# Kernel tuning notes

Measured on AMD Instinct MI355X. Metric: run time of the kernel, lower is better.

Reference implementation:

```python
import jax, jax.numpy as jnp
import numpy as np

STRIDE = 16      # image -> feature stride (224 -> 14)
POOL = 7         # ROI pool output grid
FG_HI = 0.85
FG_LO = 0.5


def setup_inputs() -> dict:
    key = jax.random.key(0)
    ks = jax.random.split(key, 8)
    B, N, M, K = 4, 128, 16, 80
    Cf, Tf, Cs, Ts, H, W = 256, 32, 2048, 8, 14, 14
    fast = jax.random.normal(ks[0], (B, Cf, Tf, H, W), jnp.float32)
    slow = jax.random.normal(ks[1], (B, Cs, Ts, H, W), jnp.float32)
    # valid gt boxes inside 224x224
    xy = jax.random.uniform(ks[2], (B, M, 2)) * 160.0
    wh = 32.0 + jax.random.uniform(ks[3], (B, M, 2)) * 48.0
    gt = jnp.concatenate([xy, xy + wh], axis=-1)
    # proposals: first M coincide with gt (guarantees IoU>=0.85 foreground), rest random
    pxy = jax.random.uniform(ks[4], (B, N - M, 2)) * 160.0
    pwh = 16.0 + jax.random.uniform(ks[5], (B, N - M, 2)) * 64.0
    props = jnp.concatenate([gt, jnp.concatenate([pxy, pxy + pwh], axis=-1)], axis=1)
    gt_classes = (jax.random.uniform(ks[6], (B, M, K)) < 0.1).astype(jnp.float32)
    C = Cf + Cs
    W_cls = jax.random.normal(ks[7], (C, K), jnp.float32) * 0.02
    b_cls = jnp.zeros((K,), jnp.float32)
    return dict(fast_feature=fast, slow_feature=slow, proposal_bboxes=props,
                gt_bboxes_batch=gt, gt_classes_batch=gt_classes,
                W_cls=W_cls, b_cls=b_cls)


def _iou(a, b):
    # a: [B,N,4], b: [B,M,4] (x1,y1,x2,y2) -> [B,N,M]
    tl = jnp.maximum(a[:, :, None, :2], b[:, None, :, :2])
    br = jnp.minimum(a[:, :, None, 2:], b[:, None, :, 2:])
    inter = jnp.prod(jnp.clip(br - tl, 0.0), axis=-1)
    area_a = jnp.prod(a[:, :, 2:] - a[:, :, :2], axis=-1)[:, :, None]
    area_b = jnp.prod(b[:, :, 2:] - b[:, :, :2], axis=-1)[:, None, :]
    return inter / (area_a + area_b - inter)


def _roi_pool(feat, boxes):
    # feat: [B,C,H,W]; boxes: [B,N,4] in image coords -> [B,N,P,P,C]
    B, C, H, W = feat.shape
    fb = boxes / STRIDE
    x1, y1, x2, y2 = fb[..., 0], fb[..., 1], fb[..., 2], fb[..., 3]
    grid = (jnp.arange(POOL, dtype=feat.dtype) + 0.5) / POOL          # [P]
    cy = y1[..., None] + grid * (y2 - y1)[..., None]                  # [B,N,P]
    cx = x1[..., None] + grid * (x2 - x1)[..., None]                  # [B,N,P]
    iy = jnp.clip(jnp.floor(cy), 0, H - 1).astype(jnp.int32)
    ix = jnp.clip(jnp.floor(cx), 0, W - 1).astype(jnp.int32)
    ft = jnp.transpose(feat, (0, 2, 3, 1))                            # [B,H,W,C]
    bidx = jnp.arange(B)[:, None, None, None]
    return ft[bidx, iy[:, :, :, None], ix[:, :, None, :]]             # [B,N,P,P,C]


def reference(fast_feature, slow_feature, proposal_bboxes, gt_bboxes_batch,
              gt_classes_batch, W_cls, b_cls):
    # temporal average pooling (AvgPool3d over full T) + channel concat, fast first
    fast = fast_feature.mean(axis=2)
    slow = slow_feature.mean(axis=2)
    feature = jnp.concatenate([fast, slow], axis=1)                   # [B,C,H,W]

    # IoU-based foreground assignment
    ious = _iou(proposal_bboxes, gt_bboxes_batch)                     # [B,N,M]
    max_ious = ious.max(axis=2)                                       # [B,N]
    assign = ious.argmax(axis=2)                                      # [B,N]
    fg_hi = max_ious >= FG_HI
    fg = jnp.where(fg_hi.any(), fg_hi, max_ious >= FG_LO)             # global fallback
    labels = jnp.take_along_axis(gt_classes_batch, assign[:, :, None], axis=1)  # [B,N,K]

    # ROI pooling (dense over all proposals; non-fg are masked out of the loss)
    pool = _roi_pool(feature, proposal_bboxes)                        # [B,N,P,P,C]
    hid = pool.mean(axis=(2, 3))                                      # [B,N,C]
    logits = jnp.einsum('bnc,ck->bnk', hid, W_cls) + b_cls            # [B,N,K]

    # multilabel soft margin loss per proposal (mean over classes)
    per = -(labels * jax.nn.log_sigmoid(logits)
            + (1.0 - labels) * jax.nn.log_sigmoid(-logits)).mean(axis=-1)  # [B,N]
    fgf = fg.astype(per.dtype)
    cnt = fgf.sum(axis=1)
    cross_entropies = jnp.where(cnt > 0, (per * fgf).sum(axis=1) / jnp.maximum(cnt, 1.0), 0.0)
    return cross_entropies  # [B]
```

## Files before the change

kernel.cpp:

```cpp
#include <hip/hip_runtime.h>
#include <math.h>

#define BB 4
#define NN 128
#define MM 16
#define KK 80
#define CF 256
#define CSL 2048
#define CT 2304
#define TFAST 32
#define TSLOW 8
#define HH 14
#define WW 14
#define HWQ 196
#define NQ4 49

#define G_OFF      0
#define G_SIZE     (BB*HWQ*KK)
#define FGF_OFF    (G_OFF + G_SIZE)
#define ASSIGN_OFF (FGF_OFF + BB*NN)
#define NUM_OFF    (ASSIGN_OFF + BB*NN)
#define CNT_OFF    (NUM_OFF + BB)
#define CTR_OFF    (CNT_OFF + BB)
#define P_OFF      (CTR_OFF + 8)

#define NSPLIT 64
#define MAXCH  43
#define P_SIZE (NSPLIT*G_SIZE)

__global__ __launch_bounds__(256) void k12_fused(const float* __restrict__ fastp,
                                                 const float* __restrict__ slowp,
                                                 const float* __restrict__ Wc,
                                                 float* __restrict__ ws,
                                                 int use_partials) {
    __shared__ float sfeat[MAXCH*HWQ + 64];
    __shared__ float sW[MAXCH*KK];
    int bid = blockIdx.x;
    int b = bid >> 6;
    int r = bid & 63;
    int gc0, nch, T, isfast;
    if (r < 16) { isfast = 1; gc0 = r * 16; nch = 16; T = TFAST; }
    else {
        int s = r - 16;
        int c0s = (s < 32) ? (43 * s) : (1376 + 42 * (s - 32));
        nch = (s < 32) ? 43 : 42;
        gc0 = CF + c0s; T = TSLOW; isfast = 0;
    }
    int tid = threadIdx.x;

    const float4* base = isfast
        ? ((const float4*)fastp + (size_t)(b * CF + gc0) * TFAST * NQ4)
        : ((const float4*)slowp + (size_t)(b * CSL + (gc0 - CF)) * TSLOW * NQ4);
    const float scale = 1.f / (float)T;
    int ntasks = nch * NQ4;
    for (int x = tid; x < ntasks; x += 256) {
        int cl = x / NQ4;
        int q  = x - cl * NQ4;
        const float4* p = base + (size_t)cl * T * NQ4 + q;
        float4 a = make_float4(0.f, 0.f, 0.f, 0.f);
        #pragma unroll 8
        for (int t = 0; t < T; ++t) {
            float4 v = p[t * NQ4];
            a.x += v.x; a.y += v.y; a.z += v.z; a.w += v.w;
        }
        a.x *= scale; a.y *= scale; a.z *= scale; a.w *= scale;
        ((float4*)sfeat)[cl * NQ4 + q] = a;
    }
    const float4* wsrc = (const float4*)Wc + (size_t)gc0 * (KK / 4);
    int wtasks = nch * (KK / 4);
    for (int x = tid; x < wtasks; x += 256) ((float4*)sW)[x] = wsrc[x];
    __syncthreads();

    int cg = tid & 31;
    int kq = tid >> 5;
    float acc[7][10];
    #pragma unroll
    for (int j = 0; j < 7; ++j)
        #pragma unroll
        for (int i = 0; i < 10; ++i) acc[j][i] = 0.f;

    const float* fr = sfeat + cg;
    const float* wr = sW + kq * 10;
    for (int c = 0; c < nch; ++c) {
        float w[10];
        #pragma unroll
        for (int i = 0; i < 10; ++i) w[i] = wr[c * KK + i];
        #pragma unroll
        for (int j = 0; j < 7; ++j) {
            float fv = fr[c * HWQ + 32 * j];
            #pragma unroll
            for (int i = 0; i < 10; ++i) acc[j][i] += fv * w[i];
        }
    }

    int k0 = kq * 10;
    if (use_partials) {
        float* P = ws + P_OFF + (size_t)r * G_SIZE + (size_t)b * (KK * HWQ);
        #pragma unroll
        for (int j = 0; j < 7; ++j) {
            int cell = cg + 32 * j;
            if (cell < HWQ) {
                #pragma unroll
                for (int i = 0; i < 10; ++i) P[(k0 + i) * HWQ + cell] = acc[j][i];
            }
        }
    } else {
        float* g = ws + G_OFF + (size_t)b * HWQ * KK;
        #pragma unroll
        for (int j = 0; j < 7; ++j) {
            int cell = cg + 32 * j;
            if (cell < HWQ) {
                #pragma unroll
                for (int i = 0; i < 10; ++i) atomicAdd(&g[cell * KK + k0 + i], acc[j][i]);
            }
        }
    }
}

__global__ __launch_bounds__(256) void kz_zero(float* __restrict__ ws) {
    int idx = blockIdx.x * 256 + threadIdx.x;
    if (idx < G_SIZE) ws[G_OFF + idx] = 0.f;
}

#define RED_BLOCKS ((G_SIZE + 511) / 512)
__global__ __launch_bounds__(512) void k2b_assign(const float* __restrict__ props,
                                                  const float* __restrict__ gtb,
                                                  float* __restrict__ ws,
                                                  int use_partials) {
    int blk = blockIdx.x;
    int t = threadIdx.x;
    if (blk < RED_BLOCKS) {
        if (!use_partials) return;
        int ridx = blk * 512 + t;
        if (ridx < G_SIZE) {
            const float* P = ws + P_OFF;
            float s = 0.f;
            #pragma unroll 16
            for (int cs = 0; cs < NSPLIT; ++cs) s += P[(size_t)cs * G_SIZE + ridx];
            int b    = ridx / (KK * HWQ);
            int rem  = ridx - b * (KK * HWQ);
            int k    = rem / HWQ;
            int cell = rem - k * HWQ;
            ws[G_OFF + (size_t)b * HWQ * KK + cell * KK + k] = s;
        }
        return;
    }
    __shared__ float sgt[BB*MM*4];
    __shared__ float sfg[BB*NN];
    __shared__ int sany;
    if (t < BB*MM*4) sgt[t] = gtb[t];
    if (t == 0) sany = 0;
    __syncthreads();
    int b = t >> 7;
    float x1 = props[t*4+0], y1 = props[t*4+1], x2 = props[t*4+2], y2 = props[t*4+3];
    float aa = (x2 - x1) * (y2 - y1);
    float best = -1.f; int arg = 0;
    for (int m = 0; m < MM; ++m) {
        const float* g = &sgt[(b*MM + m)*4];
        float tlx = fmaxf(x1, g[0]), tly = fmaxf(y1, g[1]);
        float brx = fminf(x2, g[2]), bry = fminf(y2, g[3]);
        float inter = fmaxf(brx - tlx, 0.f) * fmaxf(bry - tly, 0.f);
        float ab = (g[2] - g[0]) * (g[3] - g[1]);
        float iou = inter / (aa + ab - inter);
        if (iou > best) { best = iou; arg = m; }
    }
    if (best >= 0.85f) atomicOr(&sany, 1);
    __syncthreads();
    float fg = sany ? (best >= 0.85f ? 1.f : 0.f) : (best >= 0.5f ? 1.f : 0.f);
    sfg[t] = fg;
    ws[FGF_OFF + t] = fg;
    ((int*)ws)[ASSIGN_OFF + t] = arg;
    __syncthreads();
    if (t < BB) {
        float s = 0.f;
        for (int i = 0; i < NN; ++i) s += sfg[t*NN + i];
        ws[CNT_OFF + t] = s;
        ws[NUM_OFF + t] = 0.f;
    }
    if (t == 0) ((int*)ws)[CTR_OFF] = 0;
}

__device__ __forceinline__ float logsig(float x) {
    return fminf(x, 0.f) - log1pf(expf(-fabsf(x)));
}

__global__ __launch_bounds__(128) void k3b_loss(const float* __restrict__ props,
                                                const float* __restrict__ gtc,
                                                const float* __restrict__ bcls,
                                                float* __restrict__ ws,
                                                float* __restrict__ out) {
    int p = blockIdx.x;
    int b = p >> 7;
    int t = threadIdx.x;
    __shared__ int cells[49];
    __shared__ float red[128];
    if (ws[FGF_OFF + p] != 0.f) {
        if (t < 49) {
            int gy = t / 7, gx = t % 7;
            float x1 = props[p*4+0] * (1.f/16.f);
            float y1 = props[p*4+1] * (1.f/16.f);
            float x2 = props[p*4+2] * (1.f/16.f);
            float y2 = props[p*4+3] * (1.f/16.f);
            float gry = ((float)gy + 0.5f) / 7.f;
            float grx = ((float)gx + 0.5f) / 7.f;
            float cy = y1 + gry * (y2 - y1);
            float cx = x1 + grx * (x2 - x1);
            int iy = (int)floorf(cy); iy = min(max(iy, 0), HH-1);
            int ix = (int)floorf(cx); ix = min(max(ix, 0), WW-1);
            cells[t] = iy * WW + ix;
        }
        __syncthreads();
        float lk = 0.f;
        if (t < KK) {
            float acc = 0.f;
            const float* Gb = ws + G_OFF + b * HWQ * KK + t;
            #pragma unroll 7
            for (int g = 0; g < 49; ++g) acc += Gb[cells[g] * KK];
            float logit = acc * (1.f/49.f) + bcls[t];
            int a = ((const int*)ws)[ASSIGN_OFF + p];
            float y = gtc[(b*MM + a)*KK + t];
            lk = -(y * logsig(logit) + (1.f - y) * logsig(-logit));
        }
        red[t] = lk;
        __syncthreads();
        for (int s = 64; s > 0; s >>= 1) {
            if (t < s) red[t] += red[t + s];
            __syncthreads();
        }
        if (t == 0) atomicAdd(&ws[NUM_OFF + b], red[0] * (1.f/KK));
    }
    if (t == 0) {
        __threadfence();
        int old = atomicAdd(&((int*)ws)[CTR_OFF], 1);
        if (old == BB*NN - 1) {
            __threadfence();
            #pragma unroll
            for (int bb = 0; bb < BB; ++bb) {
                float num = atomicAdd(&ws[NUM_OFF + bb], 0.f);
                float c = ws[CNT_OFF + bb];
                out[bb] = (c > 0.f) ? num / c : 0.f;
            }
        }
    }
}

extern "C" void kernel_launch(void* const* d_in, const int* in_sizes, int n_in,
                              void* d_out, int out_size, void* d_ws, size_t ws_size,
                              hipStream_t stream) {
    const float* fastp = (const float*)d_in[0];
    const float* slowp = (const float*)d_in[1];
    const float* props = (const float*)d_in[2];
    const float* gtb   = (const float*)d_in[3];
    const float* gtc   = (const float*)d_in[4];
    const float* Wc    = (const float*)d_in[5];
    const float* bcls  = (const float*)d_in[6];
    float* ws  = (float*)d_ws;
    float* out = (float*)d_out;

    const size_t need = (size_t)(P_OFF + P_SIZE) * sizeof(float);
    const int use_partials = (ws_size >= need) ? 1 : 0;

    if (!use_partials)
        kz_zero<<<(G_SIZE + 255)/256, 256, 0, stream>>>(ws);
    k12_fused<<<BB * NSPLIT, 256, 0, stream>>>(fastp, slowp, Wc, ws, use_partials);
    k2b_assign<<<RED_BLOCKS + 1, 512, 0, stream>>>(props, gtb, ws, use_partials);
    k3b_loss<<<BB*NN, 128, 0, stream>>>(props, gtc, bcls, ws, out);
}
```

Measured before the change: 134.0 us.

## Fuse all stages into one persistent kernel with software grid barriers

```diff
diff --git a/kernel.cpp b/kernel.cpp
--- a/kernel.cpp
+++ b/kernel.cpp
@@ -27,17 +27,48 @@
 #define NSPLIT 64
 #define MAXCH  43
 #define P_SIZE (NSPLIT*G_SIZE)
-
-__global__ __launch_bounds__(256) void k12_fused(const float* __restrict__ fastp,
-                                                 const float* __restrict__ slowp,
-                                                 const float* __restrict__ Wc,
-                                                 float* __restrict__ ws,
-                                                 int use_partials) {
+#define NBLK   (BB*NSPLIT)
+
+__device__ __forceinline__ float logsig(float x) {
+    return fminf(x, 0.f) - log1pf(expf(-fabsf(x)));
+}
+
+__device__ __forceinline__ void gbarrier(int* ctr, int target) {
+    __syncthreads();
+    __threadfence();
+    __syncthreads();
+    if (threadIdx.x == 0) {
+        atomicAdd(ctr, 1);
+        while (__hip_atomic_load(ctr, __ATOMIC_RELAXED, __HIP_MEMORY_SCOPE_AGENT) < target)
+            __builtin_amdgcn_s_sleep(1);
+    }
+    __syncthreads();
+    __threadfence();
+}
+
+__global__ __launch_bounds__(256) void k_all(const float* __restrict__ fastp,
+                                             const float* __restrict__ slowp,
+                                             const float* __restrict__ Wc,
+                                             const float* __restrict__ props,
+                                             const float* __restrict__ gtb,
+                                             const float* __restrict__ gtc,
+                                             const float* __restrict__ bcls,
+                                             float* __restrict__ ws,
+                                             float* __restrict__ out) {
     __shared__ float sfeat[MAXCH*HWQ + 64];
     __shared__ float sW[MAXCH*KK];
-    int bid = blockIdx.x;
-    int b = bid >> 6;
-    int r = bid & 63;
+    __shared__ float sgt[BB*MM*4];
+    __shared__ float sfgL[BB*NN];
+    __shared__ int   sany;
+    __shared__ int   cells[49];
+    __shared__ float red[128];
+
+    int blk = blockIdx.x;
+    int tid = threadIdx.x;
+    int b = blk >> 6;
+    int r = blk & 63;
+    int* ctr = (int*)ws + CTR_OFF;
+
     int gc0, nch, T, isfast;
     if (r < 16) { isfast = 1; gc0 = r * 16; nch = 16; T = TFAST; }
     else {
@@ -46,8 +77,6 @@
         nch = (s < 32) ? 43 : 42;
         gc0 = CF + c0s; T = TSLOW; isfast = 0;
     }
-    int tid = threadIdx.x;
-
     const float4* base = isfast
         ? ((const float4*)fastp + (size_t)(b * CF + gc0) * TFAST * NQ4)
         : ((const float4*)slowp + (size_t)(b * CSL + (gc0 - CF)) * TSLOW * NQ4);
@@ -78,7 +107,6 @@
     for (int j = 0; j < 7; ++j)
         #pragma unroll
         for (int i = 0; i < 10; ++i) acc[j][i] = 0.f;
-
     const float* fr = sfeat + cg;
     const float* wr = sW + kq * 10;
     for (int c = 0; c < nch; ++c) {
@@ -92,9 +120,8 @@
             for (int i = 0; i < 10; ++i) acc[j][i] += fv * w[i];
         }
     }
-
     int k0 = kq * 10;
-    if (use_partials) {
+    {
         float* P = ws + P_OFF + (size_t)r * G_SIZE + (size_t)b * (KK * HWQ);
         #pragma unroll
         for (int j = 0; j < 7; ++j) {
@@ -104,50 +131,212 @@
                 for (int i = 0; i < 10; ++i) P[(k0 + i) * HWQ + cell] = acc[j][i];
             }
         }
-    } else {
-        float* g = ws + G_OFF + (size_t)b * HWQ * KK;
-        #pragma unroll
-        for (int j = 0; j < 7; ++j) {
-            int cell = cg + 32 * j;
-            if (cell < HWQ) {
-                #pragma unroll
-                for (int i = 0; i < 10; ++i) atomicAdd(&g[cell * KK + k0 + i], acc[j][i]);
-            }
-        }
-    }
-}
-
-__global__ __launch_bounds__(256) void kz_zero(float* __restrict__ ws) {
-    int idx = blockIdx.x * 256 + threadIdx.x;
-    if (idx < G_SIZE) ws[G_OFF + idx] = 0.f;
-}
-
-#define RED_BLOCKS ((G_SIZE + 511) / 512)
-__global__ __launch_bounds__(512) void k2b_assign(const float* __restrict__ props,
-                                                  const float* __restrict__ gtb,
-                                                  float* __restrict__ ws,
-                                                  int use_partials) {
-    int blk = blockIdx.x;
-    int t = threadIdx.x;
-    if (blk < RED_BLOCKS) {
-        if (!use_partials) return;
-        int ridx = blk * 512 + t;
+    }
+
+    if (blk == 0) {
+        if (tid < BB*MM*4) sgt[tid] = gtb[tid];
+        if (tid == 0) sany = 0;
+        __syncthreads();
+        float best2[2]; int arg2[2];
+        #pragma unroll
+        for (int it = 0; it < 2; ++it) {
+            int p = tid + 256 * it;
+            int pb = p >> 7;
+            float x1 = props[p*4+0], y1 = props[p*4+1], x2 = props[p*4+2], y2 = props[p*4+3];
+            float aa = (x2 - x1) * (y2 - y1);
+            float best = -1.f; int arg = 0;
+            for (int m = 0; m < MM; ++m) {
+                const float* g = &sgt[(pb*MM + m)*4];
+                float tlx = fmaxf(x1, g[0]), tly = fmaxf(y1, g[1]);
+                float brx = fminf(x2, g[2]), bry = fminf(y2, g[3]);
+                float inter = fmaxf(brx - tlx, 0.f) * fmaxf(bry - tly, 0.f);
+                float ab = (g[2] - g[0]) * (g[3] - g[1]);
+                float iou = inter / (aa + ab - inter);
+                if (iou > best) { best = iou; arg = m; }
+            }
+            best2[it] = best; arg2[it] = arg;
+            if (best >= 0.85f) atomicOr(&sany, 1);
+        }
+        __syncthreads();
+        int any = sany;
+        #pragma unroll
+        for (int it = 0; it < 2; ++it) {
+            int p = tid + 256 * it;
+            float fg = any ? (best2[it] >= 0.85f ? 1.f : 0.f)
+                           : (best2[it] >= 0.5f  ? 1.f : 0.f);
+            sfgL[p] = fg;
+            ws[FGF_OFF + p] = fg;
+            ((int*)ws)[ASSIGN_OFF + p] = arg2[it];
+        }
+        __syncthreads();
+        if (tid < BB) {
+            float s = 0.f;
+            for (int i = 0; i < NN; ++i) s += sfgL[tid*NN + i];
+            ws[CNT_OFF + tid] = s;
+            ws[NUM_OFF + tid] = 0.f;
+        }
+    }
+
+    gbarrier(&ctr[0], NBLK);
+
+    {
+        int ridx = blk * 256 + tid;
         if (ridx < G_SIZE) {
             const float* P = ws + P_OFF;
             float s = 0.f;
             #pragma unroll 16
             for (int cs = 0; cs < NSPLIT; ++cs) s += P[(size_t)cs * G_SIZE + ridx];
-            int b    = ridx / (KK * HWQ);
-            int rem  = ridx - b * (KK * HWQ);
+            int b2   = ridx / (KK * HWQ);
+            int rem  = ridx - b2 * (KK * HWQ);
             int k    = rem / HWQ;
             int cell = rem - k * HWQ;
-            ws[G_OFF + (size_t)b * HWQ * KK + cell * KK + k] = s;
-        }
-        return;
-    }
+            ws[G_OFF + (size_t)b2 * HWQ * KK + cell * KK + k] = s;
+        }
+    }
+
+    gbarrier(&ctr[1], NBLK);
+
+    #pragma unroll
+    for (int it = 0; it < 2; ++it) {
+        int p = blk + 256 * it;
+        int pb = p >> 7;
+        float fgp = ws[FGF_OFF + p];
+        if (fgp != 0.f) {
+            if (tid < 49) {
+                int gy = tid / 7, gx = tid % 7;
+                float x1 = props[p*4+0] * (1.f/16.f);
+                float y1 = props[p*4+1] * (1.f/16.f);
+                float x2 = props[p*4+2] * (1.f/16.f);
+                float y2 = props[p*4+3] * (1.f/16.f);
+                float gry = ((float)gy + 0.5f) / 7.f;
+                float grx = ((float)gx + 0.5f) / 7.f;
+                float cy = y1 + gry * (y2 - y1);
+                float cx = x1 + grx * (x2 - x1);
+                int iy = (int)floorf(cy); iy = min(max(iy, 0), HH-1);
+                int ix = (int)floorf(cx); ix = min(max(ix, 0), WW-1);
+                cells[tid] = iy * WW + ix;
+            }
+            __syncthreads();
+            float lk = 0.f;
+            if (tid < KK) {
+                float a = 0.f;
+                const float* Gb = ws + G_OFF + pb * HWQ * KK + tid;
+                #pragma unroll 7
+                for (int g = 0; g < 49; ++g) a += Gb[cells[g] * KK];
+                float logit = a * (1.f/49.f) + bcls[tid];
+                int asg = ((const int*)ws)[ASSIGN_OFF + p];
+                float y = gtc[(pb*MM + asg)*KK + tid];
+                lk = -(y * logsig(logit) + (1.f - y) * logsig(-logit));
+            }
+            if (tid < 128) red[tid] = (tid < KK) ? lk : 0.f;
+            __syncthreads();
+            for (int s = 64; s > 0; s >>= 1) {
+                if (tid < s) red[tid] += red[tid + s];
+                __syncthreads();
+            }
+            if (tid == 0) atomicAdd(&ws[NUM_OFF + pb], red[0] * (1.f/KK));
+            __syncthreads();
+        }
+    }
+
+    if (tid == 0) {
+        __threadfence();
+        int old = atomicAdd(&ctr[2], 1);
+        if (old == NBLK - 1) {
+            #pragma unroll
+            for (int bb = 0; bb < BB; ++bb) {
+                float num = atomicAdd(&ws[NUM_OFF + bb], 0.f);
+                float c = ws[CNT_OFF + bb];
+                out[bb] = (c > 0.f) ? num / c : 0.f;
+            }
+        }
+    }
+}
+
+__global__ __launch_bounds__(256) void kz_zero(float* __restrict__ ws) {
+    int idx = blockIdx.x * 256 + threadIdx.x;
+    if (idx < G_SIZE) ws[G_OFF + idx] = 0.f;
+}
+
+__global__ __launch_bounds__(256) void k12_atomic(const float* __restrict__ fastp,
+                                                  const float* __restrict__ slowp,
+                                                  const float* __restrict__ Wc,
+                                                  float* __restrict__ ws) {
+    __shared__ float sfeat[MAXCH*HWQ + 64];
+    __shared__ float sW[MAXCH*KK];
+    int bid = blockIdx.x;
+    int b = bid >> 6;
+    int r = bid & 63;
+    int gc0, nch, T, isfast;
+    if (r < 16) { isfast = 1; gc0 = r * 16; nch = 16; T = TFAST; }
+    else {
+        int s = r - 16;
+        int c0s = (s < 32) ? (43 * s) : (1376 + 42 * (s - 32));
+        nch = (s < 32) ? 43 : 42;
+        gc0 = CF + c0s; T = TSLOW; isfast = 0;
+    }
+    int tid = threadIdx.x;
+    const float4* base = isfast
+        ? ((const float4*)fastp + (size_t)(b * CF + gc0) * TFAST * NQ4)
+        : ((const float4*)slowp + (size_t)(b * CSL + (gc0 - CF)) * TSLOW * NQ4);
+    const float scale = 1.f / (float)T;
+    int ntasks = nch * NQ4;
+    for (int x = tid; x < ntasks; x += 256) {
+        int cl = x / NQ4;
+        int q  = x - cl * NQ4;
+        const float4* p = base + (size_t)cl * T * NQ4 + q;
+        float4 a = make_float4(0.f, 0.f, 0.f, 0.f);
+        #pragma unroll 8
+        for (int t = 0; t < T; ++t) {
+            float4 v = p[t * NQ4];
+            a.x += v.x; a.y += v.y; a.z += v.z; a.w += v.w;
+        }
+        a.x *= scale; a.y *= scale; a.z *= scale; a.w *= scale;
+        ((float4*)sfeat)[cl * NQ4 + q] = a;
+    }
+    const float4* wsrc = (const float4*)Wc + (size_t)gc0 * (KK / 4);
+    int wtasks = nch * (KK / 4);
+    for (int x = tid; x < wtasks; x += 256) ((float4*)sW)[x] = wsrc[x];
+    __syncthreads();
+    int cg = tid & 31;
+    int kq = tid >> 5;
+    float acc[7][10];
+    #pragma unroll
+    for (int j = 0; j < 7; ++j)
+        #pragma unroll
+        for (int i = 0; i < 10; ++i) acc[j][i] = 0.f;
+    const float* fr = sfeat + cg;
+    const float* wr = sW + kq * 10;
+    for (int c = 0; c < nch; ++c) {
+        float w[10];
+        #pragma unroll
+        for (int i = 0; i < 10; ++i) w[i] = wr[c * KK + i];
+        #pragma unroll
+        for (int j = 0; j < 7; ++j) {
+            float fv = fr[c * HWQ + 32 * j];
+            #pragma unroll
+            for (int i = 0; i < 10; ++i) acc[j][i] += fv * w[i];
+        }
+    }
+    int k0 = kq * 10;
+    float* g = ws + G_OFF + (size_t)b * HWQ * KK;
+    #pragma unroll
+    for (int j = 0; j < 7; ++j) {
+        int cell = cg + 32 * j;
+        if (cell < HWQ) {
+            #pragma unroll
+            for (int i = 0; i < 10; ++i) atomicAdd(&g[cell * KK + k0 + i], acc[j][i]);
+        }
+    }
+}
+
+__global__ __launch_bounds__(512) void kb_assign(const float* __restrict__ props,
+                                                 const float* __restrict__ gtb,
+                                                 float* __restrict__ ws) {
     __shared__ float sgt[BB*MM*4];
     __shared__ float sfg[BB*NN];
     __shared__ int sany;
+    int t = threadIdx.x;
     if (t < BB*MM*4) sgt[t] = gtb[t];
     if (t == 0) sany = 0;
     __syncthreads();
@@ -177,11 +366,7 @@
         ws[CNT_OFF + t] = s;
         ws[NUM_OFF + t] = 0.f;
     }
-    if (t == 0) ((int*)ws)[CTR_OFF] = 0;
-}
-
-__device__ __forceinline__ float logsig(float x) {
-    return fminf(x, 0.f) - log1pf(expf(-fabsf(x)));
+    if (t == 0) ((int*)ws)[CTR_OFF + 2] = 0;
 }
 
 __global__ __launch_bounds__(128) void k3b_loss(const float* __restrict__ props,
@@ -212,13 +397,13 @@
         __syncthreads();
         float lk = 0.f;
         if (t < KK) {
-            float acc = 0.f;
+            float a = 0.f;
             const float* Gb = ws + G_OFF + b * HWQ * KK + t;
             #pragma unroll 7
-            for (int g = 0; g < 49; ++g) acc += Gb[cells[g] * KK];
-            float logit = acc * (1.f/49.f) + bcls[t];
-            int a = ((const int*)ws)[ASSIGN_OFF + p];
-            float y = gtc[(b*MM + a)*KK + t];
+            for (int g = 0; g < 49; ++g) a += Gb[cells[g] * KK];
+            float logit = a * (1.f/49.f) + bcls[t];
+            int asg = ((const int*)ws)[ASSIGN_OFF + p];
+            float y = gtc[(b*MM + asg)*KK + t];
             lk = -(y * logsig(logit) + (1.f - y) * logsig(-logit));
         }
         red[t] = lk;
@@ -231,7 +416,7 @@
     }
     if (t == 0) {
         __threadfence();
-        int old = atomicAdd(&((int*)ws)[CTR_OFF], 1);
+        int old = atomicAdd(&((int*)ws)[CTR_OFF + 2], 1);
         if (old == BB*NN - 1) {
             __threadfence();
             #pragma unroll
@@ -260,9 +445,14 @@
     const size_t need = (size_t)(P_OFF + P_SIZE) * sizeof(float);
     const int use_partials = (ws_size >= need) ? 1 : 0;
 
-    if (!use_partials)
+    if (use_partials) {
+        hipMemsetAsync((char*)d_ws + (size_t)CTR_OFF * sizeof(float), 0,
+                       4 * sizeof(int), stream);
+        k_all<<<NBLK, 256, 0, stream>>>(fastp, slowp, Wc, props, gtb, gtc, bcls, ws, out);
+    } else {
         kz_zero<<<(G_SIZE + 255)/256, 256, 0, stream>>>(ws);
-    k12_fused<<<BB * NSPLIT, 256, 0, stream>>>(fastp, slowp, Wc, ws, use_partials);
-    k2b_assign<<<RED_BLOCKS + 1, 512, 0, stream>>>(props, gtb, ws, use_partials);
-    k3b_loss<<<BB*NN, 128, 0, stream>>>(props, gtc, bcls, ws, out);
-}
+        k12_atomic<<<BB * NSPLIT, 256, 0, stream>>>(fastp, slowp, Wc, ws);
+        kb_assign<<<1, 512, 0, stream>>>(props, gtb, ws);
+        k3b_loss<<<BB*NN, 128, 0, stream>>>(props, gtc, bcls, ws, out);
+    }
+}
```

After: 243.8 us. 1.82x slower.
